# Kernel optimization log

Measured on AMD Instinct MI355X. Metric: run time of the kernel, lower is better.

## Reference

```python
import jax, jax.numpy as jnp
import numpy as np

B, ENC_T, ENC_D = 16, 600, 512
H = 512          # hidden_size == attn_dim (Attention built with attn_dim=hidden_size)
A = 512
VOCAB = 8000
MAX_LEN = 64
SOS = 1


def setup_inputs() -> dict:
    key = jax.random.key(0)
    ks = jax.random.split(key, 16)
    n = jax.random.normal
    s = 0.04  # param init scale
    return {
        "encoder_outputs": n(ks[0], (B, ENC_T, ENC_D), dtype=jnp.float32),
        # embedding table
        "emb": n(ks[1], (VOCAB, H)) * 0.05,
        # GRU (1 layer, input = hidden + enc_dim), PyTorch layout [3H, in]/[3H, H]
        "w_ih": n(ks[2], (3 * H, H + ENC_D)) * s,
        "w_hh": n(ks[3], (3 * H, H)) * s,
        "b_ih": n(ks[4], (3 * H,)) * s,
        "b_hh": n(ks[5], (3 * H,)) * s,
        # location attention: Conv1d(1 -> A, k=3, pad=1)
        "conv_w": n(ks[6], (A, 1, 3)) * 0.1,
        "conv_b": n(ks[7], (A,)) * 0.1,
        "attn_W": n(ks[8], (A, H)) * s,      # W: dec_dim -> attn_dim, no bias
        "attn_V": n(ks[9], (A, ENC_D)) * s,  # V: enc_dim -> attn_dim, no bias
        "attn_fc_w": n(ks[10], (1, A)) * s,  # fc: attn_dim -> 1, with bias
        "attn_fc_b": n(ks[11], (1,)) * s,
        "attn_b": n(ks[12], (A,)) * s,       # extra learned bias b
        # output projection: (hidden + enc_dim) -> vocab
        "fc_w": n(ks[13], (VOCAB, H + ENC_D)) * s,
        "fc_b": n(ks[14], (VOCAB,)) * s,
    }


def reference(encoder_outputs, emb, w_ih, w_hh, b_ih, b_hh,
              conv_w, conv_b, attn_W, attn_V, attn_fc_w, attn_fc_b, attn_b,
              fc_w, fc_b):
    dt = encoder_outputs.dtype
    b, t, ed = encoder_outputs.shape
    h_dim = emb.shape[1]

    # V(values) is time-invariant across decode steps: precompute once. [B, T, A]
    Vv = jnp.einsum('btd,ad->bta', encoder_outputs, attn_V)

    tok0 = jnp.full((b,), SOS, dtype=jnp.int32)
    h0 = jnp.zeros((b, h_dim), dt)          # GRU hidden (None -> zeros)
    ctx0 = jnp.zeros((b, ed), dt)           # initial context
    aw0 = jnp.zeros((b, t), dt)             # initial attention weights

    def step(carry, _):
        tok, h, ctx, aw = carry
        # embed + concat with previous context  [B, H+E]
        x = jnp.concatenate([emb[tok], ctx], axis=-1)
        # GRU cell (PyTorch gate order r, z, n)
        gx = x @ w_ih.T + b_ih
        gh = h @ w_hh.T + b_hh
        xr, xz, xn = jnp.split(gx, 3, axis=-1)
        hr, hz, hn = jnp.split(gh, 3, axis=-1)
        r = jax.nn.sigmoid(xr + hr)
        z = jax.nn.sigmoid(xz + hz)
        ncand = jnp.tanh(xn + r * hn)
        h_new = (1.0 - z) * ncand + z * h
        # location feature: Conv1d over last attention weights. [B, A, T] -> [B, T, A]
        conv = jax.lax.conv_general_dilated(
            aw[:, None, :], conv_w, window_strides=(1,), padding=[(1, 1)],
            dimension_numbers=('NCH', 'OIH', 'NCH')) + conv_b[None, :, None]
        conv = jnp.transpose(conv, (0, 2, 1))
        # score = fc(tanh(W(q) + V(values) + conv + b))  [B, T]
        wq = h_new @ attn_W.T                      # [B, A]
        e = jnp.tanh(wq[:, None, :] + Vv + conv + attn_b)
        score = jnp.einsum('bta,a->bt', e, attn_fc_w[0]) + attn_fc_b[0]
        aw_new = jax.nn.softmax(score, axis=-1)
        # context = attn_weight @ values  [B, E]
        ctx_new = jnp.einsum('bt,btd->bd', aw_new, encoder_outputs)
        # output projection + log_softmax
        out = jnp.concatenate([h_new, ctx_new], axis=-1)
        logits = out @ fc_w.T + fc_b
        logp = jax.nn.log_softmax(logits, axis=-1)
        tok_new = jnp.argmax(logp, axis=-1).astype(jnp.int32)  # greedy symbol
        return (tok_new, h_new, ctx_new, aw_new), logp

    _, logps = jax.lax.scan(step, (tok0, h0, ctx0, aw0), None, length=MAX_LEN)
    # [T_dec, B, V] -> [B, T_dec, V], matching stacked decoder_outputs
    return jnp.transpose(logps, (1, 0, 2))
```

## Files before the change

### kernel.cpp

```cpp
#include <hip/hip_runtime.h>
#include <math.h>

#define NG 256
#define NT 512
#define XSS 516
#define NLOGW 250

__device__ __forceinline__ float ldc(const float* p) {
    return __hip_atomic_load(p, __ATOMIC_RELAXED, __HIP_MEMORY_SCOPE_AGENT);
}
__device__ __forceinline__ void stc(float* p, float v) {
    __hip_atomic_store(p, v, __ATOMIC_RELAXED, __HIP_MEMORY_SCOPE_AGENT);
}

__device__ __forceinline__ void gbar(int* cnt, int epoch, int g, int tid) {
    __syncthreads();
    if (tid == 0) {
        int* c0 = cnt + ((g & 15) << 5);
        int* c1 = cnt + 512;
        int* go = cnt + 576;
        int r = __hip_atomic_fetch_add(c0, 1, __ATOMIC_RELAXED,
                                       __HIP_MEMORY_SCOPE_AGENT);
        if (r == (epoch << 4) - 1) {
            int r2 = __hip_atomic_fetch_add(c1, 1, __ATOMIC_RELAXED,
                                            __HIP_MEMORY_SCOPE_AGENT);
            if (r2 == (epoch << 4) - 1)
                __hip_atomic_store(go, epoch, __ATOMIC_RELAXED,
                                   __HIP_MEMORY_SCOPE_AGENT);
        }
        int it = 0;
        while (__hip_atomic_load(go, __ATOMIC_RELAXED,
                                 __HIP_MEMORY_SCOPE_AGENT) < epoch) {
            if (++it > 4) __builtin_amdgcn_s_sleep(8);
        }
    }
    __syncthreads();
}

__global__ __launch_bounds__(256) void k_vv(const float* __restrict__ enc,
                                            const float* __restrict__ attn_V,
                                            float* __restrict__ Vv) {
    int wg = blockIdx.x;
    int b = wg / 40, t0 = (wg % 40) * 15;
    int tid = threadIdx.x;
    __shared__ __align__(16) float encL[15][512];
    for (int i = tid; i < 15 * 512; i += 256) {
        int tl = i >> 9, d = i & 511;
        encL[tl][d] = enc[((size_t)(b * 600) + (t0 + tl)) * 512 + d];
    }
    __syncthreads();
    for (int half = 0; half < 2; ++half) {
        int a = tid + half * 256;
        const float4* wrow = reinterpret_cast<const float4*>(attn_V + (size_t)a * 512);
        float acc[15];
#pragma unroll
        for (int tl = 0; tl < 15; ++tl) acc[tl] = 0.f;
        for (int k = 0; k < 128; ++k) {
            float4 w = wrow[k];
#pragma unroll
            for (int tl = 0; tl < 15; ++tl) {
                float4 x = reinterpret_cast<const float4*>(&encL[tl][0])[k];
                acc[tl] += w.x * x.x + w.y * x.y + w.z * x.z + w.w * x.w;
            }
        }
        for (int tl = 0; tl < 15; ++tl)
            Vv[((size_t)(b * 600) + (t0 + tl)) * 512 + a] = acc[tl];
    }
}

__global__ __launch_bounds__(NT, 1) void mega(
    const float* __restrict__ enc, const float* __restrict__ emb,
    const float* __restrict__ w_ih, const float* __restrict__ w_hh,
    const float* __restrict__ b_ih, const float* __restrict__ b_hh,
    const float* __restrict__ conv_w, const float* __restrict__ conv_b,
    const float* __restrict__ attn_W, const float* __restrict__ attn_fc_w,
    const float* __restrict__ attn_fc_b, const float* __restrict__ attn_b,
    const float* __restrict__ fc_w, const float* __restrict__ fc_b,
    const float* __restrict__ Vv,
    float* hbuf, float* ctxg, float* awg, float* scoreg, float* wqg,
    float* part, float* logZ, int* cnt, float* dout)
{
    const int g = blockIdx.x;
    const int tid = threadIdx.x;
    int epoch = 0;

    __shared__ float xs[16 * XSS];
    __shared__ float aux[2600];


    for (int s = 0; s < 64; ++s) {
        const int p = s & 1;
        if (g < 128) {
            float* pg = aux;
            float* tokf = aux + 2048;
            if (s == 0) {
                if (tid < 16) tokf[tid] = 1.0f;
                __syncthreads();
            } else {
                const int wv = tid >> 6, lane = tid & 63;
                for (int b = wv; b < 16; b += 8) {
                    float M = -3.4e38f, S = 0.f, I = 0.f;
                    for (int q = 0; q < 4; ++q) {
                        int pw = lane + (q << 6);
                        if (pw < NLOGW) {
                            const float* r = part + ((size_t)pw * 16 + b) * 4;
                            float m = ldc(r), se = ldc(r + 1), ii = ldc(r + 2);
                            if (m > M)      { S = S * expf(M - m) + se; M = m; I = ii; }
                            else if (m == M){ S += se; if (ii < I) I = ii; }
                            else            { S += se * expf(m - M); }
                        }
                    }
                    for (int off = 32; off; off >>= 1) {
                        float m  = __shfl_xor(M, off, 64);
                        float se = __shfl_xor(S, off, 64);
                        float ii = __shfl_xor(I, off, 64);
                        if (m > M)      { S = S * expf(M - m) + se; M = m; I = ii; }
                        else if (m == M){ S += se; if (ii < I) I = ii; }
                        else            { S += se * expf(m - M); }
                    }
                    if (lane == 0) {
                        tokf[b] = I;
                        if (g == 0) stc(&logZ[(s - 1) * 16 + b], M + logf(S));
                    }
                }
                __syncthreads();
            }
            const int b  = tid & 15;
            const int u  = tid >> 4;
            const int il = u & 3;
            const int pr = u >> 2;
            const int i  = (g << 2) + il;
            float ar = 0.f, az = 0.f, axn = 0.f, ahn = 0.f;
            for (int pass = 0; pass < 3; ++pass) {
                for (int idx = tid; idx < 8192; idx += NT) {
                    int bb = idx >> 9, k = idx & 511;
                    float v;
                    if (pass == 0)      v = emb[(size_t)((int)tokf[bb]) * 512 + k];
                    else if (pass == 1) v = ldc(&ctxg[(bb << 9) + k]);
                    else                v = ldc(&hbuf[((p << 4) + bb) * 512 + k]);
                    xs[bb * XSS + k] = v;
                }
                __syncthreads();
                const float* wbase = (pass == 2) ? w_hh : w_ih;
                const size_t rl = (pass == 2) ? 512 : 1024;
                const int ko = (pass == 1) ? 512 : 0;
                const float4* wr = (const float4*)(wbase + (size_t)i * rl + ko) + (pr << 4);
                const float4* wz = (const float4*)(wbase + (size_t)(512 + i) * rl + ko) + (pr << 4);
                const float4* wn = (const float4*)(wbase + (size_t)(1024 + i) * rl + ko) + (pr << 4);
                const float4* xv = (const float4*)(xs + b * XSS) + (pr << 4);
                float s0 = 0.f, s1 = 0.f, s2 = 0.f;
#pragma unroll 4
                for (int k = 0; k < 16; ++k) {
                    float4 x = xv[k];
                    float4 a = wr[k]; s0 += a.x*x.x + a.y*x.y + a.z*x.z + a.w*x.w;
                    float4 c = wz[k]; s1 += c.x*x.x + c.y*x.y + c.z*x.z + c.w*x.w;
                    float4 d = wn[k]; s2 += d.x*x.x + d.y*x.y + d.z*x.z + d.w*x.w;
                }
                ar += s0; az += s1;
                if (pass < 2) axn += s2; else ahn += s2;
                if (pass < 2) __syncthreads();
            }
            {
                int base = (((b << 2) + il) << 3) + pr;
                pg[base] = ar; pg[512 + base] = az;
                pg[1024 + base] = axn; pg[1536 + base] = ahn;
            }
            __syncthreads();
            if (tid < 64) {
                int bb = tid & 15, ill = tid >> 4;
                int ii = (g << 2) + ill;
                float sr = 0.f, sz2 = 0.f, sxn = 0.f, shn = 0.f;
                int bs = ((bb << 2) + ill) << 3;
                for (int q = 0; q < 8; ++q) {
                    sr  += pg[bs + q];        sz2 += pg[512 + bs + q];
                    sxn += pg[1024 + bs + q]; shn += pg[1536 + bs + q];
                }
                sr  += b_ih[ii] + b_hh[ii];
                sz2 += b_ih[512 + ii] + b_hh[512 + ii];
                sxn += b_ih[1024 + ii];
                shn += b_hh[1024 + ii];
                float r = 1.f / (1.f + expf(-sr));
                float z = 1.f / (1.f + expf(-sz2));
                float n = tanhf(sxn + r * shn);
                float hp = xs[bb * XSS + ii];
                stc(&hbuf[(((p ^ 1) << 4) + bb) * 512 + ii], (1.f - z) * n + z * hp);
            }
        }
        gbar(cnt, ++epoch, g, tid);

        {
            const int b = g & 15, ac = g >> 4;
            for (int idx = tid; idx < 512; idx += NT)
                xs[idx] = ldc(&hbuf[(((p ^ 1) << 4) + b) * 512 + idx]);
            __syncthreads();
            const int al = tid >> 4, ln = tid & 15;
            const int a = (ac << 5) + al;
            const float4* wr = (const float4*)(attn_W + (size_t)a * 512) + (ln << 3);
            const float4* hv = (const float4*)xs + (ln << 3);
            float acc = 0.f;
#pragma unroll
            for (int k = 0; k < 8; ++k) {
                float4 w = wr[k], x = hv[k];
                acc += w.x*x.x + w.y*x.y + w.z*x.z + w.w*x.w;
            }
            for (int off = 8; off; off >>= 1) acc += __shfl_xor(acc, off, 64);
            if (ln == 0) stc(&wqg[(b << 9) + a], acc);
        }
        gbar(cnt, ++epoch, g, tid);

        {
            const int b = g & 15, tc = g >> 4;
            const int t0 = tc * 38;
            float* wqL  = xs;
            float* cw0  = xs + 512;
            float* cw1  = xs + 1024;
            float* cw2  = xs + 1536;
            float* cbab = xs + 2048;
            float* fcwL = xs + 2560;
            for (int a = tid; a < 512; a += NT) {
                wqL[a]  = ldc(&wqg[(b << 9) + a]);
                cw0[a]  = conv_w[a * 3];
                cw1[a]  = conv_w[a * 3 + 1];
                cw2[a]  = conv_w[a * 3 + 2];
                cbab[a] = conv_b[a] + attn_b[a];
                fcwL[a] = attn_fc_w[a];
            }
            __syncthreads();
            const float fcb = attn_fc_b[0];
            const int wv = tid >> 6, lane = tid & 63;
            for (int tl = wv; tl < 38; tl += 8) {
                const int t = t0 + tl;
                if (t < 600) {
                    const float awm = (t > 0)   ? ldc(&awg[b * 600 + t - 1]) : 0.f;
                    const float aw0 = ldc(&awg[b * 600 + t]);
                    const float awp = (t < 599) ? ldc(&awg[b * 600 + t + 1]) : 0.f;
                    const float* vv = Vv + ((size_t)b * 600 + t) * 512;
                    float acc = 0.f;
#pragma unroll
                    for (int q = 0; q < 8; ++q) {
                        const int a = lane + (q << 6);
                        float uu = wqL[a] + vv[a] + cbab[a]
                                 + cw0[a] * awm + cw1[a] * aw0 + cw2[a] * awp;
                        acc += tanhf(uu) * fcwL[a];
                    }
                    for (int off = 32; off; off >>= 1) acc += __shfl_xor(acc, off, 64);
                    if (lane == 0) stc(&scoreg[b * 600 + t], acc + fcb);
                }
            }
        }
        gbar(cnt, ++epoch, g, tid);

        {
            const int b = g & 15, ec = g >> 4;
            float* pb    = xs;
            float* wredM = aux + 2064;
            float* wredS = aux + 2080;
            float* red16 = aux;
            float lm = -3.4e38f;
            for (int t = tid; t < 600; t += NT) {
                float v = ldc(&scoreg[b * 600 + t]);
                pb[t] = v;
                lm = fmaxf(lm, v);
            }
            for (int off = 32; off; off >>= 1) lm = fmaxf(lm, __shfl_xor(lm, off, 64));
            if ((tid & 63) == 0) wredM[tid >> 6] = lm;
            __syncthreads();
            float M = wredM[0];
#pragma unroll
            for (int q = 1; q < 8; ++q) M = fmaxf(M, wredM[q]);
            float lsum = 0.f;
            for (int t = tid; t < 600; t += NT) {
                float e = expf(pb[t] - M);
                pb[t] = e;
                lsum += e;
            }
            for (int off = 32; off; off >>= 1) lsum += __shfl_xor(lsum, off, 64);
            if ((tid & 63) == 0) wredS[tid >> 6] = lsum;
            __syncthreads();
            float S = 0.f;
#pragma unroll
            for (int q = 0; q < 8; ++q) S += wredS[q];
            const float invS = 1.f / S;
            if (ec == 0)
                for (int t = tid; t < 600; t += NT) stc(&awg[b * 600 + t], pb[t] * invS);
            const int tg = tid >> 5, l32 = tid & 31;
            const int e = (ec << 5) + l32;
            float acc = 0.f;
            for (int t = tg; t < 600; t += 16)
                acc += pb[t] * enc[((size_t)b * 600 + t) * 512 + e];
            red16[(tg << 5) + l32] = acc;
            __syncthreads();
            if (tg == 0) {
                float a2 = 0.f;
#pragma unroll
                for (int q = 0; q < 16; ++q) a2 += red16[(q << 5) + l32];
                stc(&ctxg[(b << 9) + e], a2 * invS);
            }
        }
        gbar(cnt, ++epoch, g, tid);

        {
            float* accL = aux;
            float acc0 = 0.f, acc1 = 0.f;
            const int bb = tid & 15, jj = (tid >> 4) & 15;
            const int act = (tid < 256);
            const int v0 = (g << 5) + (jj << 1);
            for (int pass = 0; pass < 2; ++pass) {
                for (int idx = tid; idx < 8192; idx += NT) {
                    int b2 = idx >> 9, k = idx & 511;
                    xs[b2 * XSS + k] = pass ? ldc(&ctxg[(b2 << 9) + k])
                                            : ldc(&hbuf[(((p ^ 1) << 4) + b2) * 512 + k]);
                }
                __syncthreads();
                if (g < NLOGW && act) {
                    const float4* w0 = (const float4*)(fc_w + (size_t)v0 * 1024 + (pass << 9));
                    const float4* w1 = (const float4*)(fc_w + (size_t)(v0 + 1) * 1024 + (pass << 9));
                    const float4* xv = (const float4*)(xs + bb * XSS);
#pragma unroll 4
                    for (int k = 0; k < 128; ++k) {
                        float4 x = xv[k];
                        float4 a = w0[k]; acc0 += a.x*x.x + a.y*x.y + a.z*x.z + a.w*x.w;
                        float4 c = w1[k]; acc1 += c.x*x.x + c.y*x.y + c.z*x.z + c.w*x.w;
                    }
                }
                __syncthreads();
            }
            if (g < NLOGW && act) {
                acc0 += fc_b[v0]; acc1 += fc_b[v0 + 1];
                float* o = dout + ((size_t)bb * 64 + s) * 8000;
                stc(o + v0, acc0);
                stc(o + v0 + 1, acc1);
                float bv, bi;
                if (acc0 >= acc1) { bv = acc0; bi = (float)v0; }
                else              { bv = acc1; bi = (float)(v0 + 1); }
                float se = expf(acc0 - bv) + expf(acc1 - bv);
                int rbase = (((bb << 4) + jj) << 2);
                accL[rbase] = bv; accL[rbase + 1] = bi; accL[rbase + 2] = se;
            }
            __syncthreads();
            if (g < NLOGW && tid < 16) {
                float M = -3.4e38f, I = 0.f, S = 0.f;
                for (int q = 0; q < 16; ++q) {
                    int rb = (((tid << 4) + q) << 2);
                    float m = accL[rb], ii = accL[rb + 1], se = accL[rb + 2];
                    if (m > M)      { S = S * expf(M - m) + se; M = m; I = ii; }
                    else if (m == M){ S += se; if (ii < I) I = ii; }
                    else            { S += se * expf(m - M); }
                }
                float* pr2 = part + ((size_t)g * 16 + tid) * 4;
                stc(pr2, M); stc(pr2 + 1, S); stc(pr2 + 2, I);
            }
        }
        gbar(cnt, ++epoch, g, tid);
    }

    if (g == 0) {
        const int wv = tid >> 6, lane = tid & 63;
        for (int b = wv; b < 16; b += 8) {
            float M = -3.4e38f, S = 0.f;
            for (int q = 0; q < 4; ++q) {
                int pw = lane + (q << 6);
                if (pw < NLOGW) {
                    const float* r = part + ((size_t)pw * 16 + b) * 4;
                    float m = ldc(r), se = ldc(r + 1);
                    if (m > M)      { S = S * expf(M - m) + se; M = m; }
                    else if (m == M){ S += se; }
                    else            { S += se * expf(m - M); }
                }
            }
            for (int off = 32; off; off >>= 1) {
                float m  = __shfl_xor(M, off, 64);
                float se = __shfl_xor(S, off, 64);
                if (m > M)      { S = S * expf(M - m) + se; M = m; }
                else if (m == M){ S += se; }
                else            { S += se * expf(m - M); }
            }
            if (lane == 0) stc(&logZ[63 * 16 + b], M + logf(S));
        }
    }
    gbar(cnt, ++epoch, g, tid);
    for (int r = g; r < 1024; r += NG) {
        float z = ldc(&logZ[(r & 63) * 16 + (r >> 6)]);
        float* o = dout + (size_t)r * 8000;
        for (int i = tid; i < 8000; i += NT) o[i] -= z;
    }
}

extern "C" void kernel_launch(void* const* d_in, const int* in_sizes, int n_in,
                              void* d_out, int out_size, void* d_ws, size_t ws_size,
                              hipStream_t stream) {
    const float* enc       = (const float*)d_in[0];
    const float* emb       = (const float*)d_in[1];
    const float* w_ih      = (const float*)d_in[2];
    const float* w_hh      = (const float*)d_in[3];
    const float* b_ih      = (const float*)d_in[4];
    const float* b_hh      = (const float*)d_in[5];
    const float* conv_w    = (const float*)d_in[6];
    const float* conv_b    = (const float*)d_in[7];
    const float* attn_W    = (const float*)d_in[8];
    const float* attn_V    = (const float*)d_in[9];
    const float* attn_fc_w = (const float*)d_in[10];
    const float* attn_fc_b = (const float*)d_in[11];
    const float* attn_b    = (const float*)d_in[12];
    const float* fc_w      = (const float*)d_in[13];
    const float* fc_b      = (const float*)d_in[14];

    float* ws    = (float*)d_ws;
    float* Vv    = ws;
    float* hbuf  = Vv + 4915200;
    float* ctx   = hbuf + 16384;
    float* aw    = ctx + 8192;
    float* score = aw + 9600;
    float* wq    = score + 9600;
    float* part  = wq + 8192;
    float* logZ  = part + 16384;
    int*   cnt   = (int*)(logZ + 1024);
    float* dout  = (float*)d_out;

    hipMemsetAsync(hbuf, 0, 34176 * sizeof(float), stream);
    hipMemsetAsync(cnt, 0, 1024 * sizeof(int), stream);

    k_vv<<<dim3(640), dim3(256), 0, stream>>>(enc, attn_V, Vv);

    void* args[] = {(void*)&enc, (void*)&emb, (void*)&w_ih, (void*)&w_hh,
                    (void*)&b_ih, (void*)&b_hh, (void*)&conv_w, (void*)&conv_b,
                    (void*)&attn_W, (void*)&attn_fc_w, (void*)&attn_fc_b,
                    (void*)&attn_b, (void*)&fc_w, (void*)&fc_b, (void*)&Vv,
                    (void*)&hbuf, (void*)&ctx, (void*)&aw, (void*)&score,
                    (void*)&wq, (void*)&part, (void*)&logZ, (void*)&cnt,
                    (void*)&dout};
    hipLaunchCooperativeKernel(reinterpret_cast<void*>(mega),
                               dim3(NG), dim3(NT), args, 0, stream);
}
```

Baseline: 6.548 ms.

## Replace grid barriers with per-batch barriers and hierarchical wakeup; spread GRU over all blocks

The two grid-wide barriers around the attention-score stage become barriers among only the 16 blocks that share a batch index, since those stages exchange data only within one batch row. The remaining grid barriers now use a two-level wakeup: one leader per group polls the global flag and releases its group through a group-local flag. Spin sleeps are also shortened. The GRU gate matvec now runs on all 256 blocks at two hidden units each instead of 128 blocks at four. The goal is lower barrier latency and less contention per decode step, at the cost of more counter memory and a larger memset.

```diff
diff --git a/kernel.cpp b/kernel.cpp
--- a/kernel.cpp
+++ b/kernel.cpp
@@ -13,26 +13,53 @@
     __hip_atomic_store(p, v, __ATOMIC_RELAXED, __HIP_MEMORY_SCOPE_AGENT);
 }
 
-__device__ __forceinline__ void gbar(int* cnt, int epoch, int g, int tid) {
+__device__ __forceinline__ void gbarG(int* cnt, int ge, int g, int tid) {
     __syncthreads();
     if (tid == 0) {
-        int* c0 = cnt + ((g & 15) << 5);
+        const int grp = g >> 4;
+        int* c0 = cnt + (grp << 5);
         int* c1 = cnt + 512;
-        int* go = cnt + 576;
+        int* go = cnt + 544;
+        int* wk = cnt + 576 + (grp << 5);
         int r = __hip_atomic_fetch_add(c0, 1, __ATOMIC_RELAXED,
                                        __HIP_MEMORY_SCOPE_AGENT);
-        if (r == (epoch << 4) - 1) {
+        if (r == (ge << 4) - 1) {
             int r2 = __hip_atomic_fetch_add(c1, 1, __ATOMIC_RELAXED,
                                             __HIP_MEMORY_SCOPE_AGENT);
-            if (r2 == (epoch << 4) - 1)
-                __hip_atomic_store(go, epoch, __ATOMIC_RELAXED,
+            if (r2 == (ge << 4) - 1)
+                __hip_atomic_store(go, ge, __ATOMIC_RELAXED,
                                    __HIP_MEMORY_SCOPE_AGENT);
         }
         int it = 0;
-        while (__hip_atomic_load(go, __ATOMIC_RELAXED,
-                                 __HIP_MEMORY_SCOPE_AGENT) < epoch) {
-            if (++it > 4) __builtin_amdgcn_s_sleep(8);
-        }
+        if ((g & 15) == 0) {
+            while (__hip_atomic_load(go, __ATOMIC_RELAXED,
+                                     __HIP_MEMORY_SCOPE_AGENT) < ge)
+                if (++it > 16) __builtin_amdgcn_s_sleep(1);
+            __hip_atomic_store(wk, ge, __ATOMIC_RELAXED,
+                               __HIP_MEMORY_SCOPE_AGENT);
+        } else {
+            while (__hip_atomic_load(wk, __ATOMIC_RELAXED,
+                                     __HIP_MEMORY_SCOPE_AGENT) < ge)
+                if (++it > 16) __builtin_amdgcn_s_sleep(1);
+        }
+    }
+    __syncthreads();
+}
+
+__device__ __forceinline__ void gbarS(int* cnt, int se, int b, int tid) {
+    __syncthreads();
+    if (tid == 0) {
+        int* cs = cnt + 1088 + (b << 5);
+        int* gs = cnt + 1600 + (b << 5);
+        int r = __hip_atomic_fetch_add(cs, 1, __ATOMIC_RELAXED,
+                                       __HIP_MEMORY_SCOPE_AGENT);
+        if (r == (se << 4) - 1)
+            __hip_atomic_store(gs, se, __ATOMIC_RELAXED,
+                               __HIP_MEMORY_SCOPE_AGENT);
+        int it = 0;
+        while (__hip_atomic_load(gs, __ATOMIC_RELAXED,
+                                 __HIP_MEMORY_SCOPE_AGENT) < se)
+            if (++it > 16) __builtin_amdgcn_s_sleep(1);
     }
     __syncthreads();
 }
@@ -82,15 +109,15 @@
 {
     const int g = blockIdx.x;
     const int tid = threadIdx.x;
-    int epoch = 0;
+    const int bg = g & 15;
+    int ge = 0, se = 0;
 
     __shared__ float xs[16 * XSS];
     __shared__ float aux[2600];
 
-
     for (int s = 0; s < 64; ++s) {
         const int p = s & 1;
-        if (g < 128) {
+        {
             float* pg = aux;
             float* tokf = aux + 2048;
             if (s == 0) {
@@ -104,19 +131,19 @@
                         int pw = lane + (q << 6);
                         if (pw < NLOGW) {
                             const float* r = part + ((size_t)pw * 16 + b) * 4;
-                            float m = ldc(r), se = ldc(r + 1), ii = ldc(r + 2);
-                            if (m > M)      { S = S * expf(M - m) + se; M = m; I = ii; }
-                            else if (m == M){ S += se; if (ii < I) I = ii; }
-                            else            { S += se * expf(m - M); }
+                            float m = ldc(r), se2 = ldc(r + 1), ii = ldc(r + 2);
+                            if (m > M)      { S = S * expf(M - m) + se2; M = m; I = ii; }
+                            else if (m == M){ S += se2; if (ii < I) I = ii; }
+                            else            { S += se2 * expf(m - M); }
                         }
                     }
                     for (int off = 32; off; off >>= 1) {
                         float m  = __shfl_xor(M, off, 64);
-                        float se = __shfl_xor(S, off, 64);
+                        float se2 = __shfl_xor(S, off, 64);
                         float ii = __shfl_xor(I, off, 64);
-                        if (m > M)      { S = S * expf(M - m) + se; M = m; I = ii; }
-                        else if (m == M){ S += se; if (ii < I) I = ii; }
-                        else            { S += se * expf(m - M); }
+                        if (m > M)      { S = S * expf(M - m) + se2; M = m; I = ii; }
+                        else if (m == M){ S += se2; if (ii < I) I = ii; }
+                        else            { S += se2 * expf(m - M); }
                     }
                     if (lane == 0) {
                         tokf[b] = I;
@@ -127,9 +154,9 @@
             }
             const int b  = tid & 15;
             const int u  = tid >> 4;
-            const int il = u & 3;
-            const int pr = u >> 2;
-            const int i  = (g << 2) + il;
+            const int il = u & 1;
+            const int pr = u >> 1;
+            const int i  = (g << 1) + il;
             float ar = 0.f, az = 0.f, axn = 0.f, ahn = 0.f;
             for (int pass = 0; pass < 3; ++pass) {
                 for (int idx = tid; idx < 8192; idx += NT) {
@@ -144,13 +171,13 @@
                 const float* wbase = (pass == 2) ? w_hh : w_ih;
                 const size_t rl = (pass == 2) ? 512 : 1024;
                 const int ko = (pass == 1) ? 512 : 0;
-                const float4* wr = (const float4*)(wbase + (size_t)i * rl + ko) + (pr << 4);
-                const float4* wz = (const float4*)(wbase + (size_t)(512 + i) * rl + ko) + (pr << 4);
-                const float4* wn = (const float4*)(wbase + (size_t)(1024 + i) * rl + ko) + (pr << 4);
-                const float4* xv = (const float4*)(xs + b * XSS) + (pr << 4);
+                const float4* wr = (const float4*)(wbase + (size_t)i * rl + ko) + (pr << 3);
+                const float4* wz = (const float4*)(wbase + (size_t)(512 + i) * rl + ko) + (pr << 3);
+                const float4* wn = (const float4*)(wbase + (size_t)(1024 + i) * rl + ko) + (pr << 3);
+                const float4* xv = (const float4*)(xs + b * XSS) + (pr << 3);
                 float s0 = 0.f, s1 = 0.f, s2 = 0.f;
-#pragma unroll 4
-                for (int k = 0; k < 16; ++k) {
+#pragma unroll
+                for (int k = 0; k < 8; ++k) {
                     float4 x = xv[k];
                     float4 a = wr[k]; s0 += a.x*x.x + a.y*x.y + a.z*x.z + a.w*x.w;
                     float4 c = wz[k]; s1 += c.x*x.x + c.y*x.y + c.z*x.z + c.w*x.w;
@@ -161,17 +188,17 @@
                 if (pass < 2) __syncthreads();
             }
             {
-                int base = (((b << 2) + il) << 3) + pr;
+                int base = (((b << 1) + il) << 4) + pr;
                 pg[base] = ar; pg[512 + base] = az;
                 pg[1024 + base] = axn; pg[1536 + base] = ahn;
             }
             __syncthreads();
-            if (tid < 64) {
+            if (tid < 32) {
                 int bb = tid & 15, ill = tid >> 4;
-                int ii = (g << 2) + ill;
+                int ii = (g << 1) + ill;
                 float sr = 0.f, sz2 = 0.f, sxn = 0.f, shn = 0.f;
-                int bs = ((bb << 2) + ill) << 3;
-                for (int q = 0; q < 8; ++q) {
+                int bs = ((bb << 1) + ill) << 4;
+                for (int q = 0; q < 16; ++q) {
                     sr  += pg[bs + q];        sz2 += pg[512 + bs + q];
                     sxn += pg[1024 + bs + q]; shn += pg[1536 + bs + q];
                 }
@@ -186,12 +213,12 @@
                 stc(&hbuf[(((p ^ 1) << 4) + bb) * 512 + ii], (1.f - z) * n + z * hp);
             }
         }
-        gbar(cnt, ++epoch, g, tid);
+        gbarG(cnt, ++ge, g, tid);
 
         {
-            const int b = g & 15, ac = g >> 4;
+            const int ac = g >> 4;
             for (int idx = tid; idx < 512; idx += NT)
-                xs[idx] = ldc(&hbuf[(((p ^ 1) << 4) + b) * 512 + idx]);
+                xs[idx] = ldc(&hbuf[(((p ^ 1) << 4) + bg) * 512 + idx]);
             __syncthreads();
             const int al = tid >> 4, ln = tid & 15;
             const int a = (ac << 5) + al;
@@ -204,12 +231,12 @@
                 acc += w.x*x.x + w.y*x.y + w.z*x.z + w.w*x.w;
             }
             for (int off = 8; off; off >>= 1) acc += __shfl_xor(acc, off, 64);
-            if (ln == 0) stc(&wqg[(b << 9) + a], acc);
-        }
-        gbar(cnt, ++epoch, g, tid);
+            if (ln == 0) stc(&wqg[(bg << 9) + a], acc);
+        }
+        gbarS(cnt, ++se, bg, tid);
 
         {
-            const int b = g & 15, tc = g >> 4;
+            const int tc = g >> 4;
             const int t0 = tc * 38;
             float* wqL  = xs;
             float* cw0  = xs + 512;
@@ -218,7 +245,7 @@
             float* cbab = xs + 2048;
             float* fcwL = xs + 2560;
             for (int a = tid; a < 512; a += NT) {
-                wqL[a]  = ldc(&wqg[(b << 9) + a]);
+                wqL[a]  = ldc(&wqg[(bg << 9) + a]);
                 cw0[a]  = conv_w[a * 3];
                 cw1[a]  = conv_w[a * 3 + 1];
                 cw2[a]  = conv_w[a * 3 + 2];
@@ -231,10 +258,10 @@
             for (int tl = wv; tl < 38; tl += 8) {
                 const int t = t0 + tl;
                 if (t < 600) {
-                    const float awm = (t > 0)   ? ldc(&awg[b * 600 + t - 1]) : 0.f;
-                    const float aw0 = ldc(&awg[b * 600 + t]);
-                    const float awp = (t < 599) ? ldc(&awg[b * 600 + t + 1]) : 0.f;
-                    const float* vv = Vv + ((size_t)b * 600 + t) * 512;
+                    const float awm = (t > 0)   ? ldc(&awg[bg * 600 + t - 1]) : 0.f;
+                    const float aw0 = ldc(&awg[bg * 600 + t]);
+                    const float awp = (t < 599) ? ldc(&awg[bg * 600 + t + 1]) : 0.f;
+                    const float* vv = Vv + ((size_t)bg * 600 + t) * 512;
                     float acc = 0.f;
 #pragma unroll
                     for (int q = 0; q < 8; ++q) {
@@ -244,21 +271,21 @@
                         acc += tanhf(uu) * fcwL[a];
                     }
                     for (int off = 32; off; off >>= 1) acc += __shfl_xor(acc, off, 64);
-                    if (lane == 0) stc(&scoreg[b * 600 + t], acc + fcb);
-                }
-            }
-        }
-        gbar(cnt, ++epoch, g, tid);
+                    if (lane == 0) stc(&scoreg[bg * 600 + t], acc + fcb);
+                }
+            }
+        }
+        gbarS(cnt, ++se, bg, tid);
 
         {
-            const int b = g & 15, ec = g >> 4;
+            const int ec = g >> 4;
             float* pb    = xs;
             float* wredM = aux + 2064;
             float* wredS = aux + 2080;
             float* red16 = aux;
             float lm = -3.4e38f;
             for (int t = tid; t < 600; t += NT) {
-                float v = ldc(&scoreg[b * 600 + t]);
+                float v = ldc(&scoreg[bg * 600 + t]);
                 pb[t] = v;
                 lm = fmaxf(lm, v);
             }
@@ -282,22 +309,22 @@
             for (int q = 0; q < 8; ++q) S += wredS[q];
             const float invS = 1.f / S;
             if (ec == 0)
-                for (int t = tid; t < 600; t += NT) stc(&awg[b * 600 + t], pb[t] * invS);
+                for (int t = tid; t < 600; t += NT) stc(&awg[bg * 600 + t], pb[t] * invS);
             const int tg = tid >> 5, l32 = tid & 31;
             const int e = (ec << 5) + l32;
             float acc = 0.f;
             for (int t = tg; t < 600; t += 16)
-                acc += pb[t] * enc[((size_t)b * 600 + t) * 512 + e];
+                acc += pb[t] * enc[((size_t)bg * 600 + t) * 512 + e];
             red16[(tg << 5) + l32] = acc;
             __syncthreads();
             if (tg == 0) {
                 float a2 = 0.f;
 #pragma unroll
                 for (int q = 0; q < 16; ++q) a2 += red16[(q << 5) + l32];
-                stc(&ctxg[(b << 9) + e], a2 * invS);
-            }
-        }
-        gbar(cnt, ++epoch, g, tid);
+                stc(&ctxg[(bg << 9) + e], a2 * invS);
+            }
+        }
+        gbarG(cnt, ++ge, g, tid);
 
         {
             float* accL = aux;
@@ -333,25 +360,25 @@
                 float bv, bi;
                 if (acc0 >= acc1) { bv = acc0; bi = (float)v0; }
                 else              { bv = acc1; bi = (float)(v0 + 1); }
-                float se = expf(acc0 - bv) + expf(acc1 - bv);
+                float se2 = expf(acc0 - bv) + expf(acc1 - bv);
                 int rbase = (((bb << 4) + jj) << 2);
-                accL[rbase] = bv; accL[rbase + 1] = bi; accL[rbase + 2] = se;
+                accL[rbase] = bv; accL[rbase + 1] = bi; accL[rbase + 2] = se2;
             }
             __syncthreads();
             if (g < NLOGW && tid < 16) {
                 float M = -3.4e38f, I = 0.f, S = 0.f;
                 for (int q = 0; q < 16; ++q) {
                     int rb = (((tid << 4) + q) << 2);
-                    float m = accL[rb], ii = accL[rb + 1], se = accL[rb + 2];
-                    if (m > M)      { S = S * expf(M - m) + se; M = m; I = ii; }
-                    else if (m == M){ S += se; if (ii < I) I = ii; }
-                    else            { S += se * expf(m - M); }
+                    float m = accL[rb], ii = accL[rb + 1], se2 = accL[rb + 2];
+                    if (m > M)      { S = S * expf(M - m) + se2; M = m; I = ii; }
+                    else if (m == M){ S += se2; if (ii < I) I = ii; }
+                    else            { S += se2 * expf(m - M); }
                 }
                 float* pr2 = part + ((size_t)g * 16 + tid) * 4;
                 stc(pr2, M); stc(pr2 + 1, S); stc(pr2 + 2, I);
             }
         }
-        gbar(cnt, ++epoch, g, tid);
+        gbarG(cnt, ++ge, g, tid);
     }
 
     if (g == 0) {
@@ -362,23 +389,23 @@
                 int pw = lane + (q << 6);
                 if (pw < NLOGW) {
                     const float* r = part + ((size_t)pw * 16 + b) * 4;
-                    float m = ldc(r), se = ldc(r + 1);
-                    if (m > M)      { S = S * expf(M - m) + se; M = m; }
-                    else if (m == M){ S += se; }
-                    else            { S += se * expf(m - M); }
+                    float m = ldc(r), se2 = ldc(r + 1);
+                    if (m > M)      { S = S * expf(M - m) + se2; M = m; }
+                    else if (m == M){ S += se2; }
+                    else            { S += se2 * expf(m - M); }
                 }
             }
             for (int off = 32; off; off >>= 1) {
                 float m  = __shfl_xor(M, off, 64);
-                float se = __shfl_xor(S, off, 64);
-                if (m > M)      { S = S * expf(M - m) + se; M = m; }
-                else if (m == M){ S += se; }
-                else            { S += se * expf(m - M); }
+                float se2 = __shfl_xor(S, off, 64);
+                if (m > M)      { S = S * expf(M - m) + se2; M = m; }
+                else if (m == M){ S += se2; }
+                else            { S += se2 * expf(m - M); }
             }
             if (lane == 0) stc(&logZ[63 * 16 + b], M + logf(S));
         }
     }
-    gbar(cnt, ++epoch, g, tid);
+    gbarG(cnt, ++ge, g, tid);
     for (int r = g; r < 1024; r += NG) {
         float z = ldc(&logZ[(r & 63) * 16 + (r >> 6)]);
         float* o = dout + (size_t)r * 8000;
@@ -418,7 +445,7 @@
     float* dout  = (float*)d_out;
 
     hipMemsetAsync(hbuf, 0, 34176 * sizeof(float), stream);
-    hipMemsetAsync(cnt, 0, 1024 * sizeof(int), stream);
+    hipMemsetAsync(cnt, 0, 4096 * sizeof(int), stream);
 
     k_vv<<<dim3(640), dim3(256), 0, stream>>>(enc, attn_V, Vv);
 
```

After: 6.938 ms. +6.0%, slower.
